# Kernel tuning notes

Hardware: AMD Instinct MI355X
Metric: run time of the kernel (lower is better)

Reference implementation:

```python
import jax, jax.numpy as jnp
import numpy as np

B = 8192      # batch
LAT = 256     # latent_dimension
HID = 512     # hidden_size
INP = 128     # input_size (n_layer_types + 1 feature)
T = 64        # max_length
MLP = 512     # fixed MLP width in source


def _lin(key, fan_in, fan_out):
    kw, kb = jax.random.split(key)
    s = 1.0 / np.sqrt(fan_in)
    W = jax.random.uniform(kw, (fan_in, fan_out), jnp.float32, -s, s)
    b = jax.random.uniform(kb, (fan_out,), jnp.float32, -s, s)
    return W, b


def setup_inputs() -> dict:
    key = jax.random.key(0)
    ks = jax.random.split(key, 16)
    x = jax.random.normal(ks[0], (B, LAT), jnp.float32)
    W1, b1 = _lin(ks[1], LAT, MLP)
    W2, b2 = _lin(ks[2], MLP, MLP)
    W3, b3 = _lin(ks[3], MLP, MLP)
    Wh1, bh1 = _lin(ks[4], MLP, MLP)
    Wh2, bh2 = _lin(ks[5], MLP, HID)
    Wc1, bc1 = _lin(ks[6], MLP, MLP)
    Wc2, bc2 = _lin(ks[7], MLP, HID)
    Wx1, bx1 = _lin(ks[8], MLP, MLP)
    Wx2, bx2 = _lin(ks[9], MLP, INP)
    Wih, bih = _lin(ks[10], INP, 4 * HID)   # LSTM input->gates (i,f,g,o)
    Whh, bhh = _lin(ks[11], HID, 4 * HID)   # LSTM hidden->gates
    Wp, bp = _lin(ks[12], HID, INP)          # predictor head
    return dict(x=x, W1=W1, b1=b1, W2=W2, b2=b2, W3=W3, b3=b3,
                Wh1=Wh1, bh1=bh1, Wh2=Wh2, bh2=bh2,
                Wc1=Wc1, bc1=bc1, Wc2=Wc2, bc2=bc2,
                Wx1=Wx1, bx1=bx1, Wx2=Wx2, bx2=bx2,
                Wih=Wih, bih=bih, Whh=Whh, bhh=bhh, Wp=Wp, bp=bp)


def _lrelu(v):
    return jnp.where(v >= 0, v, 0.2 * v)


def _head(v):
    # split [d-1, 1]: softmax over layer types, sigmoid on feature scalar
    lt = jax.nn.softmax(v[..., :-1], axis=-1)
    ft = jax.nn.sigmoid(v[..., -1:])
    return jnp.concatenate([lt, ft], axis=-1)


def reference(x, W1, b1, W2, b2, W3, b3, Wh1, bh1, Wh2, bh2,
              Wc1, bc1, Wc2, bc2, Wx1, bx1, Wx2, bx2,
              Wih, bih, Whh, bhh, Wp, bp):
    z = _lrelu(x @ W1 + b1)
    z = _lrelu(z @ W2 + b2)
    z = _lrelu(z @ W3 + b3)
    h = _lrelu(z @ Wh1 + bh1) @ Wh2 + bh2          # [B, HID]
    c = _lrelu(z @ Wc1 + bc1) @ Wc2 + bc2          # [B, HID]
    x0 = _head(_lrelu(z @ Wx1 + bx1) @ Wx2 + bx2)  # [B, INP]

    def step(carry, _):
        xt, h, c = carry
        g = xt @ Wih + h @ Whh + (bih + bhh)        # [B, 4*HID]
        i, f, gg, o = jnp.split(g, 4, axis=-1)      # torch gate order i,f,g,o
        c2 = jax.nn.sigmoid(f) * c + jax.nn.sigmoid(i) * jnp.tanh(gg)
        h2 = jax.nn.sigmoid(o) * jnp.tanh(c2)
        nxt = _head(h2 @ Wp + bp)
        return (nxt, h2, c2), nxt

    # The torch loop reruns the LSTM over the growing prefix with the same
    # initial (h,c) and takes the last output; by LSTM causality this equals
    _, ys = jax.lax.scan(step, (x0, h, c), None, length=T)
    return jnp.transpose(ys, (1, 0, 2))  # [B, T, INP]
```

## Files before the change

### kernel.cpp

```cpp
#include <hip/hip_runtime.h>


typedef _Float16 h16;
typedef __attribute__((ext_vector_type(8))) _Float16 f16x8;
typedef __attribute__((ext_vector_type(4))) float f32x4;

#define BB 8192
#define TT 64

__device__ __forceinline__ void gload16(const void* g, void* lds) {
  __builtin_amdgcn_global_load_lds(
      (const __attribute__((address_space(1))) unsigned int*)g,
      (__attribute__((address_space(3))) unsigned int*)lds, 16, 0, 0);
}

__device__ __forceinline__ float sigm(float x) { return 1.f / (1.f + __expf(-x)); }
__device__ __forceinline__ float tanhf_(float x) { return 2.f / (1.f + __expf(-2.f * x)) - 1.f; }

#define MIDBAR_LG()                                        \
  do {                                                     \
    __builtin_amdgcn_s_barrier();                          \
    asm volatile("s_waitcnt lgkmcnt(0)" ::: "memory");     \
    __builtin_amdgcn_sched_barrier(0);                     \
  } while (0)
#define ENDBAR()                                           \
  do {                                                     \
    __builtin_amdgcn_s_barrier();                          \
    asm volatile("" ::: "memory");                         \
  } while (0)

__global__ __launch_bounds__(512, 2) void gate8(
    const h16* __restrict__ A, const h16* __restrict__ Bt,
    const float* __restrict__ bg, float* __restrict__ Cbuf,
    h16* __restrict__ Hout) {
  __shared__ __align__(16) h16 As[2][16384];
  __shared__ __align__(16) h16 Bs[2][16384];
  const int tid = threadIdx.x;
  const int lane = tid & 63;
  const int wid = tid >> 6;
  const int wr = wid >> 2, wc = wid & 3;
  const int m0 = blockIdx.x * 256;
  const int n0 = blockIdx.y * 256;
  const int arow = lane & 15, khi = lane >> 4;
  const int x7 = arow & 7;

  auto stage = [&](h16(*dst)[16384], int slot, int h, const h16* src, int base,
                   int kt) {
#pragma unroll
    for (int li = 0; li < 2; ++li) {
      int rowbase = li * 128 + h * 64 + wid * 8;
      int row = rowbase + (lane >> 3);
      int gc = (lane & 7) ^ (lane >> 3);
      gload16(src + (size_t)(base + row) * 640 + kt * 64 + gc * 8,
              &dst[slot][rowbase * 64]);
    }
  };

  f32x4 acc[8][4];
#pragma unroll
  for (int i = 0; i < 8; ++i)
#pragma unroll
    for (int jj = 0; jj < 4; ++jj) acc[i][jj] = (f32x4)0.f;
  f16x8 af[4], bf[2][4];

  auto readA = [&](int slot, int ms, int ks) {
#pragma unroll
    for (int mr = 0; mr < 4; ++mr) {
      int r = wr * 128 + ms * 64 + mr * 16 + arow;
      af[mr] = *(const f16x8*)&As[slot][r * 64 + ((ks * 4 + khi) ^ x7) * 8];
    }
  };
  auto readB = [&](int slot, int ks) {
#pragma unroll
    for (int jj = 0; jj < 4; ++jj) {
      int rb = wc * 64 + jj * 16 + arow;
      bf[ks][jj] = *(const f16x8*)&Bs[slot][rb * 64 + ((ks * 4 + khi) ^ x7) * 8];
    }
  };
  auto mfma16 = [&](int ms, int ks) {
    __builtin_amdgcn_s_setprio(1);
#pragma unroll
    for (int mr = 0; mr < 4; ++mr)
#pragma unroll
      for (int jj = 0; jj < 4; ++jj)
        acc[ms * 4 + mr][jj] = __builtin_amdgcn_mfma_f32_16x16x32_f16(
            af[mr], bf[ks][jj], acc[ms * 4 + mr][jj], 0, 0, 0);
    __builtin_amdgcn_s_setprio(0);
  };

  stage(Bs, 0, 0, Bt, n0, 0);
  stage(Bs, 0, 1, Bt, n0, 0);
  stage(As, 0, 0, A, m0, 0);
  stage(As, 0, 1, A, m0, 0);
  stage(Bs, 1, 0, Bt, n0, 1);
  stage(Bs, 1, 1, Bt, n0, 1);
  stage(As, 1, 0, A, m0, 1);
  asm volatile("s_waitcnt vmcnt(6)" ::: "memory");
  ENDBAR();

#pragma unroll 1
  for (int i = 0; i < 5; ++i) {
    const int t2 = 2 * i + 2, t3 = 2 * i + 3;
    readB(0, 0);
    readB(0, 1);
    readA(0, 0, 0);
    stage(As, 1, 1, A, m0, 2 * i + 1);
    MIDBAR_LG();
    mfma16(0, 0);
    ENDBAR();
    readA(0, 0, 1);
    if (t2 < 10) stage(Bs, 0, 0, Bt, n0, t2);
    MIDBAR_LG();
    mfma16(0, 1);
    ENDBAR();
    readA(0, 1, 0);
    if (t2 < 10) stage(Bs, 0, 1, Bt, n0, t2);
    MIDBAR_LG();
    mfma16(1, 0);
    ENDBAR();
    readA(0, 1, 1);
    if (t2 < 10) stage(As, 0, 0, A, m0, t2);
    if (i < 4)
      asm volatile("s_waitcnt vmcnt(6)" ::: "memory");
    else
      asm volatile("s_waitcnt vmcnt(0)" ::: "memory");
    MIDBAR_LG();
    mfma16(1, 1);
    ENDBAR();
    readB(1, 0);
    readB(1, 1);
    readA(1, 0, 0);
    if (t2 < 10) stage(As, 0, 1, A, m0, t2);
    MIDBAR_LG();
    mfma16(0, 0);
    ENDBAR();
    readA(1, 0, 1);
    if (t3 < 10) stage(Bs, 1, 0, Bt, n0, t3);
    MIDBAR_LG();
    mfma16(0, 1);
    ENDBAR();
    readA(1, 1, 0);
    if (t3 < 10) stage(Bs, 1, 1, Bt, n0, t3);
    MIDBAR_LG();
    mfma16(1, 0);
    ENDBAR();
    readA(1, 1, 1);
    if (t3 < 10) stage(As, 1, 0, A, m0, t3);
    if (i < 4)
      asm volatile("s_waitcnt vmcnt(6)" ::: "memory");
    else
      asm volatile("s_waitcnt vmcnt(0)" ::: "memory");
    MIDBAR_LG();
    mfma16(1, 1);
    ENDBAR();
  }

  const int nb = n0 + wc * 64;
  const float bI = bg[nb + arow];
  const float bF = bg[nb + 16 + arow];
  const float bG = bg[nb + 32 + arow];
  const float bO = bg[nb + 48 + arow];
  const int hj = blockIdx.y * 64 + wc * 16 + arow;
#pragma unroll
  for (int mrep = 0; mrep < 8; ++mrep) {
#pragma unroll
    for (int r = 0; r < 4; ++r) {
      int m = m0 + wr * 128 + mrep * 16 + khi * 4 + r;
      float gi = sigm(acc[mrep][0][r] + bI);
      float gf = sigm(acc[mrep][1][r] + bF);
      float gg = tanhf_(acc[mrep][2][r] + bG);
      float go = sigm(acc[mrep][3][r] + bO);
      size_t ci = (size_t)m * 512 + hj;
      float c2 = gf * Cbuf[ci] + gi * gg;
      Cbuf[ci] = c2;
      Hout[(size_t)m * 640 + 128 + hj] = (h16)(go * tanhf_(c2));
    }
  }
}

__global__ __launch_bounds__(256) void head256(
    const h16* __restrict__ A, int lda, const h16* __restrict__ Bt,
    const float* __restrict__ bias, int nkt, h16* __restrict__ Xout,
    float* __restrict__ ydst, int tstep, int swz) {
  __shared__ __align__(16) h16 As[2][32 * 64];
  __shared__ __align__(16) h16 Bs[2][128 * 64];
  __shared__ float lgs[32 * 132];
  const int tid = threadIdx.x;
  const int lane = tid & 63;
  const int w = tid >> 6;
  const int rs = w & 1, ch = w >> 1;
  const int arow = lane & 15, khi = lane >> 4;
  const int x7 = arow & 7;

  int bid = blockIdx.x;
  int m0;
  if (swz) {
    int g = bid & 7, k = bid >> 3;
    m0 = (g + 8 * (k & 3)) * 256 + (k >> 2) * 32;
  } else {
    m0 = bid * 32;
  }

  auto stageA = [&](int slot, int kt) {
    int rowbase = w * 8;
    int gc = (lane & 7) ^ (lane >> 3);
    int row = rowbase + (lane >> 3);
    gload16(A + (size_t)(m0 + row) * lda + kt * 64 + gc * 8,
            &As[slot][rowbase * 64]);
  };
  auto stageB = [&](int slot, int kt) {
#pragma unroll
    for (int li = 0; li < 4; ++li) {
      int rowbase = li * 32 + w * 8;
      int row = rowbase + (lane >> 3);
      int gc = (lane & 7) ^ (lane >> 3);
      gload16(Bt + (size_t)row * 512 + kt * 64 + gc * 8, &Bs[slot][rowbase * 64]);
    }
  };

  f32x4 acc[4];
#pragma unroll
  for (int j = 0; j < 4; ++j) acc[j] = (f32x4)0.f;

  stageA(0, 0);
  stageB(0, 0);
#pragma unroll 1
  for (int kt = 0; kt < nkt; ++kt) {
    int p = kt & 1;
    if (kt + 1 < nkt) {
      stageA(p ^ 1, kt + 1);
      stageB(p ^ 1, kt + 1);
      asm volatile("s_waitcnt vmcnt(5)" ::: "memory");
    } else {
      asm volatile("s_waitcnt vmcnt(0)" ::: "memory");
    }
    ENDBAR();
#pragma unroll
    for (int kk = 0; kk < 2; ++kk) {
      int kc = kk * 4 + khi;
      int ra = rs * 16 + arow;
      f16x8 afr = *(const f16x8*)&As[p][ra * 64 + (kc ^ x7) * 8];
#pragma unroll
      for (int j = 0; j < 4; ++j) {
        int rb = (ch * 4 + j) * 16 + arow;
        f16x8 bfr = *(const f16x8*)&Bs[p][rb * 64 + (kc ^ x7) * 8];
        acc[j] = __builtin_amdgcn_mfma_f32_16x16x32_f16(afr, bfr, acc[j], 0, 0, 0);
      }
    }
    ENDBAR();
  }

#pragma unroll
  for (int j = 0; j < 4; ++j)
#pragma unroll
    for (int r = 0; r < 4; ++r)
      lgs[(rs * 16 + khi * 4 + r) * 132 + (ch * 4 + j) * 16 + arow] = acc[j][r];
  __syncthreads();
  {
    int row = tid >> 3, g8 = tid & 7;
    float v[16];
    float mx = -1e30f;
#pragma unroll
    for (int q = 0; q < 16; ++q) {
      int col = g8 * 16 + q;
      v[q] = lgs[row * 132 + col] + bias[col];
      if (col != 127) mx = fmaxf(mx, v[q]);
    }
#pragma unroll
    for (int s = 1; s < 8; s <<= 1) mx = fmaxf(mx, __shfl_xor(mx, s, 8));
    float sm = 0.f;
#pragma unroll
    for (int q = 0; q < 16; ++q) {
      int col = g8 * 16 + q;
      if (col != 127) sm += __expf(v[q] - mx);
    }
#pragma unroll
    for (int s = 1; s < 8; s <<= 1) sm += __shfl_xor(sm, s, 8);
    float inv = 1.f / sm;
    h16 xo[16];
    float yo[16];
#pragma unroll
    for (int q = 0; q < 16; ++q) {
      int col = g8 * 16 + q;
      float res = (col == 127) ? sigm(v[q]) : __expf(v[q] - mx) * inv;
      xo[q] = (h16)res;
      yo[q] = res;
    }
    h16* xd = Xout + (size_t)(m0 + row) * 640 + g8 * 16;
    *(f16x8*)xd = *(f16x8*)&xo[0];
    *(f16x8*)(xd + 8) = *(f16x8*)&xo[8];
    if (ydst) {
      float* yd = ydst + ((size_t)(m0 + row) * 64 + tstep) * 128 + g8 * 16;
#pragma unroll
      for (int q = 0; q < 4; ++q) *(f32x4*)(yd + 4 * q) = *(f32x4*)&yo[4 * q];
    }
  }
}

enum { EP_LRELU = 0, EP_LIN16 = 1, EP_F32 = 2 };

template <int EP>
__global__ __launch_bounds__(256) void gemm128(
    const h16* __restrict__ A, int lda, const h16* __restrict__ Bt,
    const float* __restrict__ bias, int K, h16* __restrict__ out16, int ldo,
    int ocol, float* __restrict__ outf, int ldf) {
  __shared__ __align__(16) h16 As[128 * 64];
  __shared__ __align__(16) h16 Bs[128 * 64];
  const int tid = threadIdx.x;
  const int lane = tid & 63;
  const int w = tid >> 6;
  const int m0 = blockIdx.x * 128;
  const int n0 = blockIdx.y * 128;

  f32x4 acc[4][4];
#pragma unroll
  for (int i = 0; i < 4; ++i)
#pragma unroll
    for (int jj = 0; jj < 4; ++jj) acc[i][jj] = (f32x4)0.f;

  const int rh = (w >> 1) * 64;
  const int arow = lane & 15;
  const int khi = lane >> 4;

  const int nkt = K >> 6;
  for (int kt = 0; kt < nkt; ++kt) {
#pragma unroll
    for (int li = 0; li < 4; ++li) {
      int L = w * 4 + li;
      int r = L * 8 + (lane >> 3);
      int c = lane & 7;
      int gc = c ^ (r & 7);
      gload16(A + (size_t)(m0 + r) * lda + kt * 64 + gc * 8, &As[L * 512]);
      gload16(Bt + (size_t)(n0 + r) * K + kt * 64 + gc * 8, &Bs[L * 512]);
    }
    __syncthreads();
#pragma unroll
    for (int kk = 0; kk < 2; ++kk) {
      const int kc = kk * 4 + khi;
      f16x8 af[4], bf[4];
#pragma unroll
      for (int mt = 0; mt < 4; ++mt) {
        int r = rh + mt * 16 + arow;
        af[mt] = *(const f16x8*)&As[r * 64 + (kc ^ (r & 7)) * 8];
      }
#pragma unroll
      for (int jj = 0; jj < 4; ++jj) {
        int nt = (w & 1) * 4 + jj;
        int r = nt * 16 + arow;
        bf[jj] = *(const f16x8*)&Bs[r * 64 + (kc ^ (r & 7)) * 8];
      }
#pragma unroll
      for (int mt = 0; mt < 4; ++mt)
#pragma unroll
        for (int jj = 0; jj < 4; ++jj)
          acc[mt][jj] =
              __builtin_amdgcn_mfma_f32_16x16x32_f16(af[mt], bf[jj], acc[mt][jj], 0, 0, 0);
    }
    __syncthreads();
  }

#pragma unroll
  for (int mt = 0; mt < 4; ++mt) {
#pragma unroll
    for (int jj = 0; jj < 4; ++jj) {
      int nt = (w & 1) * 4 + jj;
      int n = n0 + nt * 16 + arow;
      float bv = bias[n];
#pragma unroll
      for (int r = 0; r < 4; ++r) {
        int m = m0 + rh + mt * 16 + khi * 4 + r;
        float v = acc[mt][jj][r] + bv;
        if constexpr (EP == EP_LRELU) {
          v = v >= 0.f ? v : 0.2f * v;
          out16[(size_t)m * ldo + n] = (h16)v;
        } else if constexpr (EP == EP_LIN16) {
          out16[(size_t)m * ldo + ocol + n] = (h16)v;
        } else {
          outf[(size_t)m * ldf + n] = v;
        }
      }
    }
  }
}

__global__ void cvt16(const float* __restrict__ in, h16* __restrict__ out, int n) {
  int i = blockIdx.x * 256 + threadIdx.x;
  if (i < n) out[i] = (h16)in[i];
}

__global__ void transposeW(const float* __restrict__ W, h16* __restrict__ WT, int K,
                           int N) {
  int i = blockIdx.x * 256 + threadIdx.x;
  if (i >= K * N) return;
  int k = i / N, n = i % N;
  WT[(size_t)n * K + k] = (h16)W[i];
}

__global__ void prep_gate(const float* __restrict__ Wih, const float* __restrict__ Whh,
                          const float* __restrict__ bih, const float* __restrict__ bhh,
                          h16* __restrict__ WgT, float* __restrict__ bg) {
  int i = blockIdx.x * 256 + threadIdx.x;
  if (i >= 2048 * 640) return;
  int np = i / 640, k = i % 640;
  int by = np >> 8, wcc = (np >> 6) & 3, q = (np >> 4) & 3, jj = np & 15;
  int orig = q * 512 + by * 64 + wcc * 16 + jj;
  float wv = (k < 128) ? Wih[(size_t)k * 2048 + orig]
                       : Whh[(size_t)(k - 128) * 2048 + orig];
  WgT[i] = (h16)wv;
  if (k == 0) bg[np] = bih[orig] + bhh[orig];
}

extern "C" void kernel_launch(void* const* d_in, const int* in_sizes, int n_in,
                              void* d_out, int out_size, void* d_ws, size_t ws_size,
                              hipStream_t stream) {
  const float* x = (const float*)d_in[0];
  const float* W1 = (const float*)d_in[1];
  const float* b1 = (const float*)d_in[2];
  const float* W2 = (const float*)d_in[3];
  const float* b2 = (const float*)d_in[4];
  const float* W3 = (const float*)d_in[5];
  const float* b3 = (const float*)d_in[6];
  const float* Wh1 = (const float*)d_in[7];
  const float* bh1 = (const float*)d_in[8];
  const float* Wh2 = (const float*)d_in[9];
  const float* bh2 = (const float*)d_in[10];
  const float* Wc1 = (const float*)d_in[11];
  const float* bc1 = (const float*)d_in[12];
  const float* Wc2 = (const float*)d_in[13];
  const float* bc2 = (const float*)d_in[14];
  const float* Wx1 = (const float*)d_in[15];
  const float* bx1 = (const float*)d_in[16];
  const float* Wx2 = (const float*)d_in[17];
  const float* bx2 = (const float*)d_in[18];
  const float* Wih = (const float*)d_in[19];
  const float* bih = (const float*)d_in[20];
  const float* Whh = (const float*)d_in[21];
  const float* bhh = (const float*)d_in[22];
  const float* Wp = (const float*)d_in[23];
  const float* bp = (const float*)d_in[24];

  char* ws = (char*)d_ws;
  size_t off = 0;
  auto take = [&](size_t bytes) -> void* {
    void* p = ws + off;
    off += (bytes + 255) & ~(size_t)255;
    return p;
  };
  h16* X16 = (h16*)take((size_t)BB * 256 * 2);
  h16* Za = (h16*)take((size_t)BB * 512 * 2);
  h16* Zb = (h16*)take((size_t)BB * 512 * 2);
  h16* XHa = (h16*)take((size_t)BB * 640 * 2);
  h16* XHb = (h16*)take((size_t)BB * 640 * 2);
  float* C = (float*)take((size_t)BB * 512 * 4);
  h16* W1T = (h16*)take(256 * 512 * 2);
  h16* W2T = (h16*)take(512 * 512 * 2);
  h16* W3T = (h16*)take(512 * 512 * 2);
  h16* Wh1T = (h16*)take(512 * 512 * 2);
  h16* Wh2T = (h16*)take(512 * 512 * 2);
  h16* Wc1T = (h16*)take(512 * 512 * 2);
  h16* Wc2T = (h16*)take(512 * 512 * 2);
  h16* Wx1T = (h16*)take(512 * 512 * 2);
  h16* Wx2T = (h16*)take(128 * 512 * 2);
  h16* WpT = (h16*)take(128 * 512 * 2);
  h16* WgT = (h16*)take((size_t)2048 * 640 * 2);
  float* bg = (float*)take(2048 * 4);

  dim3 blk(256);
  cvt16<<<(BB * 256 + 255) / 256, blk, 0, stream>>>(x, X16, BB * 256);
  transposeW<<<(256 * 512 + 255) / 256, blk, 0, stream>>>(W1, W1T, 256, 512);
  transposeW<<<(512 * 512 + 255) / 256, blk, 0, stream>>>(W2, W2T, 512, 512);
  transposeW<<<(512 * 512 + 255) / 256, blk, 0, stream>>>(W3, W3T, 512, 512);
  transposeW<<<(512 * 512 + 255) / 256, blk, 0, stream>>>(Wh1, Wh1T, 512, 512);
  transposeW<<<(512 * 512 + 255) / 256, blk, 0, stream>>>(Wh2, Wh2T, 512, 512);
  transposeW<<<(512 * 512 + 255) / 256, blk, 0, stream>>>(Wc1, Wc1T, 512, 512);
  transposeW<<<(512 * 512 + 255) / 256, blk, 0, stream>>>(Wc2, Wc2T, 512, 512);
  transposeW<<<(512 * 512 + 255) / 256, blk, 0, stream>>>(Wx1, Wx1T, 512, 512);
  transposeW<<<(512 * 128 + 255) / 256, blk, 0, stream>>>(Wx2, Wx2T, 512, 128);
  transposeW<<<(512 * 128 + 255) / 256, blk, 0, stream>>>(Wp, WpT, 512, 128);
  prep_gate<<<(2048 * 640 + 255) / 256, blk, 0, stream>>>(Wih, Whh, bih, bhh, WgT, bg);

  gemm128<EP_LRELU><<<dim3(64, 4), blk, 0, stream>>>(X16, 256, W1T, b1, 256, Za, 512, 0, nullptr, 0);
  gemm128<EP_LRELU><<<dim3(64, 4), blk, 0, stream>>>(Za, 512, W2T, b2, 512, Zb, 512, 0, nullptr, 0);
  gemm128<EP_LRELU><<<dim3(64, 4), blk, 0, stream>>>(Zb, 512, W3T, b3, 512, Za, 512, 0, nullptr, 0);
  gemm128<EP_LRELU><<<dim3(64, 4), blk, 0, stream>>>(Za, 512, Wh1T, bh1, 512, Zb, 512, 0, nullptr, 0);
  gemm128<EP_LIN16><<<dim3(64, 4), blk, 0, stream>>>(Zb, 512, Wh2T, bh2, 512, XHa, 640, 128, nullptr, 0);
  gemm128<EP_LRELU><<<dim3(64, 4), blk, 0, stream>>>(Za, 512, Wc1T, bc1, 512, Zb, 512, 0, nullptr, 0);
  gemm128<EP_F32><<<dim3(64, 4), blk, 0, stream>>>(Zb, 512, Wc2T, bc2, 512, nullptr, 0, 0, C, 512);
  gemm128<EP_LRELU><<<dim3(64, 4), blk, 0, stream>>>(Za, 512, Wx1T, bx1, 512, Zb, 512, 0, nullptr, 0);
  head256<<<256, blk, 0, stream>>>(Zb, 512, Wx2T, bx2, 8, XHa, nullptr, 0, 0);

  float* yout = (float*)d_out;
  for (int t = 0; t < TT; ++t) {
    h16* in_ = (t & 1) ? XHb : XHa;
    h16* out_ = (t & 1) ? XHa : XHb;
    gate8<<<dim3(32, 8), dim3(512), 0, stream>>>(in_, WgT, bg, C, out_);
    head256<<<256, blk, 0, stream>>>(out_ + 128, 640, WpT, bp, 8, out_, yout, t, 1);
  }
}
```

Before: 2.839 ms.

## Fuse predictor head into LSTM gate kernel via per-row-block atomic counters

Removes the separate head256 launch per timestep by having each gate8 block, after writing its h slice, wait on an atomic counter until all 8 column-blocks of its 256-row tile are done. Each block then computes the 128-wide predictor head, softmax and sigmoid for a 32-row subset, writing the next input and the output. This saves 64 kernel launches and a global round trip. The cost is a spin-wait inside the kernel that assumes all 8 column blocks of a row tile are co-resident, which risks deadlock or stalls if they are not scheduled together.

```diff
diff --git a/kernel.cpp b/kernel.cpp
--- a/kernel.cpp
+++ b/kernel.cpp
@@ -32,7 +32,9 @@
 __global__ __launch_bounds__(512, 2) void gate8(
     const h16* __restrict__ A, const h16* __restrict__ Bt,
     const float* __restrict__ bg, float* __restrict__ Cbuf,
-    h16* __restrict__ Hout) {
+    h16* __restrict__ Hout, const h16* __restrict__ WpT,
+    const float* __restrict__ bp, float* __restrict__ yout, int tstep,
+    unsigned int* __restrict__ hc) {
   __shared__ __align__(16) h16 As[2][16384];
   __shared__ __align__(16) h16 Bs[2][16384];
   const int tid = threadIdx.x;
@@ -155,26 +157,148 @@
     ENDBAR();
   }
 
-  const int nb = n0 + wc * 64;
-  const float bI = bg[nb + arow];
-  const float bF = bg[nb + 16 + arow];
-  const float bG = bg[nb + 32 + arow];
-  const float bO = bg[nb + 48 + arow];
-  const int hj = blockIdx.y * 64 + wc * 16 + arow;
-#pragma unroll
-  for (int mrep = 0; mrep < 8; ++mrep) {
-#pragma unroll
-    for (int r = 0; r < 4; ++r) {
-      int m = m0 + wr * 128 + mrep * 16 + khi * 4 + r;
-      float gi = sigm(acc[mrep][0][r] + bI);
-      float gf = sigm(acc[mrep][1][r] + bF);
-      float gg = tanhf_(acc[mrep][2][r] + bG);
-      float go = sigm(acc[mrep][3][r] + bO);
-      size_t ci = (size_t)m * 512 + hj;
-      float c2 = gf * Cbuf[ci] + gi * gg;
-      Cbuf[ci] = c2;
-      Hout[(size_t)m * 640 + 128 + hj] = (h16)(go * tanhf_(c2));
-    }
+  {
+    const int nb = n0 + wc * 64;
+    const float bI = bg[nb + arow];
+    const float bF = bg[nb + 16 + arow];
+    const float bG = bg[nb + 32 + arow];
+    const float bO = bg[nb + 48 + arow];
+    const int hj = blockIdx.y * 64 + wc * 16 + arow;
+#pragma unroll
+    for (int mrep = 0; mrep < 8; ++mrep) {
+#pragma unroll
+      for (int r = 0; r < 4; ++r) {
+        int m = m0 + wr * 128 + mrep * 16 + khi * 4 + r;
+        float gi = sigm(acc[mrep][0][r] + bI);
+        float gf = sigm(acc[mrep][1][r] + bF);
+        float gg = tanhf_(acc[mrep][2][r] + bG);
+        float go = sigm(acc[mrep][3][r] + bO);
+        size_t ci = (size_t)m * 512 + hj;
+        float c2 = gf * Cbuf[ci] + gi * gg;
+        Cbuf[ci] = c2;
+        Hout[(size_t)m * 640 + 128 + hj] = (h16)(go * tanhf_(c2));
+      }
+    }
+  }
+
+  h16* Ws0 = &As[0][0];
+  h16* Ws1 = &As[0][8192];
+  h16* Hs0 = &As[1][0];
+  h16* Hs1 = &As[1][2048];
+  float* lgs = (float*)&As[1][4096];
+
+  const int hr0 = m0 + blockIdx.y * 32;
+
+  auto stageW = [&](h16* dst, int kt) {
+#pragma unroll
+    for (int li = 0; li < 2; ++li) {
+      int rowbase = wid * 16 + li * 8;
+      int row = rowbase + (lane >> 3);
+      int gc = (lane & 7) ^ (lane >> 3);
+      gload16(WpT + (size_t)row * 512 + kt * 64 + gc * 8, dst + rowbase * 64);
+    }
+  };
+  auto stageH = [&](h16* dst, int kt) {
+    int rowbase = (wid & 3) * 8;
+    int row = rowbase + (lane >> 3);
+    int gc = (lane & 7) ^ (lane >> 3);
+    gload16(Hout + (size_t)(hr0 + row) * 640 + 128 + kt * 64 + gc * 8,
+            dst + rowbase * 64);
+  };
+
+  __syncthreads();
+  if (tid == 0)
+    (void)__hip_atomic_fetch_add(&hc[blockIdx.x], 1u, __ATOMIC_ACQ_REL,
+                                 __HIP_MEMORY_SCOPE_AGENT);
+  stageW(Ws0, 0);
+  stageW(Ws1, 1);
+  if (tid == 0) {
+    while (__hip_atomic_load(&hc[blockIdx.x], __ATOMIC_RELAXED,
+                             __HIP_MEMORY_SCOPE_AGENT) < 8u)
+      __builtin_amdgcn_s_sleep(1);
+  }
+  __syncthreads();
+  asm volatile("s_waitcnt vmcnt(0)" ::: "memory");
+  __scoped_atomic_thread_fence(__ATOMIC_ACQUIRE, __MEMORY_SCOPE_DEVICE);
+
+  const int rs = wid & 1;
+  const int ch = wid >> 1;
+  f32x4 hacc[2] = {(f32x4)0.f, (f32x4)0.f};
+
+  stageH(Hs0, 0);
+  stageH(Hs1, 1);
+#pragma unroll 1
+  for (int kt = 0; kt < 8; ++kt) {
+    h16* Wp_ = (kt & 1) ? Ws1 : Ws0;
+    h16* Hp_ = (kt & 1) ? Hs1 : Hs0;
+    if (kt == 0)
+      asm volatile("s_waitcnt vmcnt(1)" ::: "memory");
+    else if (kt < 7)
+      asm volatile("s_waitcnt vmcnt(3)" ::: "memory");
+    else
+      asm volatile("s_waitcnt vmcnt(0)" ::: "memory");
+    __syncthreads();
+    {
+      int ra = rs * 16 + arow;
+#pragma unroll
+      for (int kk = 0; kk < 2; ++kk) {
+        f16x8 afr = *(const f16x8*)&Hp_[ra * 64 + ((kk * 4 + khi) ^ (ra & 7)) * 8];
+#pragma unroll
+        for (int j = 0; j < 2; ++j) {
+          int rb = (ch * 2 + j) * 16 + arow;
+          f16x8 bfr =
+              *(const f16x8*)&Wp_[rb * 64 + ((kk * 4 + khi) ^ (rb & 7)) * 8];
+          hacc[j] = __builtin_amdgcn_mfma_f32_16x16x32_f16(afr, bfr, hacc[j], 0, 0, 0);
+        }
+      }
+    }
+    __syncthreads();
+    if (kt + 2 < 8) {
+      stageW(Wp_, kt + 2);
+      stageH(Hp_, kt + 2);
+    }
+  }
+
+#pragma unroll
+  for (int j = 0; j < 2; ++j)
+#pragma unroll
+    for (int r = 0; r < 4; ++r)
+      lgs[(rs * 16 + khi * 4 + r) * 132 + (ch * 2 + j) * 16 + arow] = hacc[j][r];
+  __syncthreads();
+  {
+    int row = tid >> 4, cg = tid & 15;
+    float v[8];
+    float mx = -1e30f;
+#pragma unroll
+    for (int q = 0; q < 8; ++q) {
+      int col = cg * 8 + q;
+      v[q] = lgs[row * 132 + col] + bp[col];
+      if (col != 127) mx = fmaxf(mx, v[q]);
+    }
+#pragma unroll
+    for (int s = 1; s < 16; s <<= 1) mx = fmaxf(mx, __shfl_xor(mx, s, 16));
+    float sm = 0.f;
+#pragma unroll
+    for (int q = 0; q < 8; ++q) {
+      int col = cg * 8 + q;
+      if (col != 127) sm += __expf(v[q] - mx);
+    }
+#pragma unroll
+    for (int s = 1; s < 16; s <<= 1) sm += __shfl_xor(sm, s, 16);
+    float inv = 1.f / sm;
+    h16 xo[8];
+    float yo[8];
+#pragma unroll
+    for (int q = 0; q < 8; ++q) {
+      int col = cg * 8 + q;
+      float res = (col == 127) ? sigm(v[q]) : __expf(v[q] - mx) * inv;
+      xo[q] = (h16)res;
+      yo[q] = res;
+    }
+    *(f16x8*)&Hout[(size_t)(hr0 + row) * 640 + cg * 8] = *(f16x8*)xo;
+    float* yd = yout + ((size_t)(hr0 + row) * 64 + tstep) * 128 + cg * 8;
+    *(f32x4*)yd = *(f32x4*)&yo[0];
+    *(f32x4*)(yd + 4) = *(f32x4*)&yo[4];
   }
 }
 
@@ -464,6 +588,9 @@
   h16* WpT = (h16*)take(128 * 512 * 2);
   h16* WgT = (h16*)take((size_t)2048 * 640 * 2);
   float* bg = (float*)take(2048 * 4);
+  unsigned int* hcnt = (unsigned int*)take((size_t)TT * 32 * 4);
+
+  (void)hipMemsetAsync(hcnt, 0, (size_t)TT * 32 * 4, stream);
 
   dim3 blk(256);
   cvt16<<<(BB * 256 + 255) / 256, blk, 0, stream>>>(x, X16, BB * 256);
@@ -493,7 +620,7 @@
   for (int t = 0; t < TT; ++t) {
     h16* in_ = (t & 1) ? XHb : XHa;
     h16* out_ = (t & 1) ? XHa : XHb;
-    gate8<<<dim3(32, 8), dim3(512), 0, stream>>>(in_, WgT, bg, C, out_);
-    head256<<<256, blk, 0, stream>>>(out_ + 128, 640, WpT, bp, 8, out_, yout, t, 1);
-  }
-}
+    gate8<<<dim3(32, 8), dim3(512), 0, stream>>>(in_, WgT, bg, C, out_, WpT, bp,
+                                                 yout, t, hcnt + t * 32);
+  }
+}
```

Result: slower. 3.970 ms (+39.8%).
